# Kernel tuning notes

Hardware: AMD Instinct MI355X
Metric: run time of the kernel (lower is better)

## Reference

```python
import jax, jax.numpy as jnp
import numpy as np

N_ROIS, ROI_DIM, D, H, L, FF, NCLS = 200, 199, 192, 6, 3, 576, 2
EPS = 1e-5

def _ln(x, g, b):
    m = jnp.mean(x, axis=-1, keepdims=True)
    v = jnp.mean((x - m) ** 2, axis=-1, keepdims=True)
    return (x - m) * jax.lax.rsqrt(v + EPS) * g + b

def _gelu(x):
    return jax.nn.gelu(x, approximate=False)

def _mha(q, k, v, Wqkv, bqkv, Wo, bo):
    # q: [B,Q,D], k/v: [B,S,D]; Wqkv: [3,D,D], bqkv: [3,D]
    B, Q, _ = q.shape
    S = k.shape[1]
    Dh = D // H
    qp = (q @ Wqkv[0] + bqkv[0]).reshape(B, Q, H, Dh)
    kp = (k @ Wqkv[1] + bqkv[1]).reshape(B, S, H, Dh)
    vp = (v @ Wqkv[2] + bqkv[2]).reshape(B, S, H, Dh)
    scores = jnp.einsum('bqhd,bkhd->bhqk', qp, kp) / jnp.sqrt(jnp.float32(Dh))
    attn = jax.nn.softmax(scores, axis=-1)
    out = jnp.einsum('bhqk,bkhd->bqhd', attn, vp).reshape(B, Q, D)
    return out @ Wo + bo

def setup_inputs() -> dict:
    key = jax.random.key(0)
    ks = iter(jax.random.split(key, 40))
    r = lambda *s: jax.random.normal(next(ks), s, dtype=jnp.float32) * 0.02
    inp = {
        'x': jax.random.normal(next(ks), (256, N_ROIS * ROI_DIM), dtype=jnp.float32),
        # 200 distinct per-ROI tokenizers, stacked for a single batched GEMM
        'roi_W': r(N_ROIS, ROI_DIM, D), 'roi_b': r(N_ROIS, D),
        'roi_ln_g': jnp.ones((N_ROIS, D), jnp.float32), 'roi_ln_b': jnp.zeros((N_ROIS, D), jnp.float32),
        'pos_emb': r(N_ROIS, D),
        # encoder layers stacked on leading L dim
        'enc_Wqkv': r(L, 3, D, D), 'enc_bqkv': r(L, 3, D),
        'enc_Wo': r(L, D, D), 'enc_bo': r(L, D),
        'enc_ln1_g': jnp.ones((L, D), jnp.float32), 'enc_ln1_b': jnp.zeros((L, D), jnp.float32),
        'enc_W1': r(L, D, FF), 'enc_b1': r(L, FF),
        'enc_W2': r(L, FF, D), 'enc_b2': r(L, D),
        'enc_ln2_g': jnp.ones((L, D), jnp.float32), 'enc_ln2_b': jnp.zeros((L, D), jnp.float32),
        # attention pooling MHA
        'pool_Wqkv': r(3, D, D), 'pool_bqkv': r(3, D),
        'pool_Wo': r(D, D), 'pool_bo': r(D),
        # classifier head
        'cls_ln_g': jnp.ones((D,), jnp.float32), 'cls_ln_b': jnp.zeros((D,), jnp.float32),
        'cls_W1': r(D, D // 2), 'cls_b1': r(D // 2),
        'cls_W2': r(D // 2, D // 4), 'cls_b2': r(D // 4),
        'cls_W3': r(D // 4, NCLS), 'cls_b3': r(NCLS),
    }
    return inp

def reference(x, roi_W, roi_b, roi_ln_g, roi_ln_b, pos_emb,
              enc_Wqkv, enc_bqkv, enc_Wo, enc_bo, enc_ln1_g, enc_ln1_b,
              enc_W1, enc_b1, enc_W2, enc_b2, enc_ln2_g, enc_ln2_b,
              pool_Wqkv, pool_bqkv, pool_Wo, pool_bo,
              cls_ln_g, cls_ln_b, cls_W1, cls_b1, cls_W2, cls_b2, cls_W3, cls_b3):
    B = x.shape[0]
    roi = x.reshape(B, N_ROIS, ROI_DIM)
    # fused per-ROI Linear (200 distinct weights) as one batched GEMM
    tok = jnp.einsum('brf,rfd->brd', roi, roi_W) + roi_b  # [B,200,192]
    tok = _gelu(_ln(tok, roi_ln_g, roi_ln_b))  # dropout = identity (eval)
    tok = tok + pos_emb[None]
    # post-norm transformer encoder (PyTorch default norm_first=False)
    h = tok
    for i in range(L):
        a = _mha(h, h, h, enc_Wqkv[i], enc_bqkv[i], enc_Wo[i], enc_bo[i])
        h = _ln(h + a, enc_ln1_g[i], enc_ln1_b[i])
        f = _gelu(h @ enc_W1[i] + enc_b1[i]) @ enc_W2[i] + enc_b2[i]
        h = _ln(h + f, enc_ln2_g[i], enc_ln2_b[i])
    # MHA pooling: query = mean over ROI tokens
    q = jnp.mean(h, axis=1, keepdims=True)  # [B,1,D]
    pooled = _mha(q, h, h, pool_Wqkv, pool_bqkv, pool_Wo, pool_bo)[:, 0]  # [B,D]
    # classifier
    z = _ln(pooled, cls_ln_g, cls_ln_b)
    z = _gelu(z @ cls_W1 + cls_b1)
    z = _gelu(z @ cls_W2 + cls_b2)
    return z @ cls_W3 + cls_b3
```

## Files before the change

### kernel.cpp

```cpp
#include <hip/hip_runtime.h>
#include <math.h>


typedef unsigned short u16;
typedef unsigned int u32;
typedef __attribute__((ext_vector_type(8))) __bf16 bf16x8;
typedef __attribute__((ext_vector_type(4))) float f32x4;

#define GLL16(gp, lp) __builtin_amdgcn_global_load_lds(                 \
    (const __attribute__((address_space(1))) void*)(gp),                \
    (__attribute__((address_space(3))) void*)(lp), 16, 0, 0)

#define FENCE_VM()   do { asm volatile("s_waitcnt vmcnt(0)" ::: "memory");  \
                          __builtin_amdgcn_sched_barrier(0); } while (0)
#define FENCE_LGKM() do { asm volatile("s_waitcnt lgkmcnt(0)" ::: "memory");\
                          __builtin_amdgcn_sched_barrier(0); } while (0)

__device__ __forceinline__ u16 f2bf(float x) {
    u32 u = __float_as_uint(x);
    u = (u + 0x7FFFu + ((u >> 16) & 1u)) >> 16;
    return (u16)u;
}
__device__ __forceinline__ float bf2f(u16 h) {
    return __uint_as_float(((u32)h) << 16);
}

__device__ __forceinline__ float gelu_exact(float x) {
    return 0.5f * x * (1.0f + erff(x * 0.7071067811865475f));
}

__device__ __forceinline__ float wave_sum(float v) {
#pragma unroll
    for (int o = 32; o > 0; o >>= 1) v += __shfl_xor(v, o, 64);
    return v;
}
__device__ __forceinline__ float wave_max(float v) {
#pragma unroll
    for (int o = 32; o > 0; o >>= 1) v = fmaxf(v, __shfl_xor(v, o, 64));
    return v;
}
__device__ __forceinline__ float row_sum16(float v) {
    v += __shfl_xor(v, 1, 64); v += __shfl_xor(v, 2, 64);
    v += __shfl_xor(v, 4, 64); v += __shfl_xor(v, 8, 64);
    return v;
}

__device__ __forceinline__ f32x4 mfma_bf16(bf16x8 a, bf16x8 b, f32x4 c) {
    return __builtin_amdgcn_mfma_f32_16x16x32_bf16(a, b, c, 0, 0, 0);
}

__global__ void conv_wt(const float* __restrict__ W, u16* __restrict__ oh,
                        int K, int N)
{
    const long z = blockIdx.z;
    const int idx = blockIdx.x * 256 + threadIdx.x;
    if (idx >= K * N) return;
    const int k = idx / N, n = idx - k * N;
    const float x = W[z * K * N + idx];
    oh[z * (long)K * N + (long)n * K + k] = f2bf(x);
}

__global__ void conv_x(const float* __restrict__ x, u16* __restrict__ xh)
{
    const long idx = (long)blockIdx.x * 256 + threadIdx.x;
    if (idx >= 200L * 256 * 224) return;
    const int k = (int)(idx % 224);
    const long t = idx / 224;
    const int m = (int)(t % 256);
    const int z = (int)(t / 256);
    const float v = (k < 199) ? x[(long)m * 39800 + z * 199 + k] : 0.f;
    xh[idx] = f2bf(v);
}

__global__ void conv_roiw(const float* __restrict__ W, u16* __restrict__ oh)
{
    __shared__ float tile[32][33];
    const int z = blockIdx.z;
    const int k0 = blockIdx.x * 32;
    const int n0 = blockIdx.y * 32;
    for (int i = threadIdx.y; i < 32; i += 8) {
        const int k = k0 + i, n = n0 + threadIdx.x;
        tile[i][threadIdx.x] = (k < 199) ? W[((long)z * 199 + k) * 192 + n] : 0.f;
    }
    __syncthreads();
    for (int i = threadIdx.y; i < 32; i += 8) {
        const int n = n0 + i, k = k0 + threadIdx.x;
        const float v = tile[threadIdx.x][i];
        oh[((long)z * 192 + n) * 224 + k] = f2bf(v);
    }
}

template<int EPI>
__global__ __launch_bounds__(256, 3) void gemm_ns(
    const u16* __restrict__ Ah,
    const u16* __restrict__ Bh,
    const float* __restrict__ bias,
    float* __restrict__ C, u16* __restrict__ Ch,
    int N, int K)
{
    __shared__ u16 Ash[128][32];
    __shared__ u16 Bsh[192][32];

    const int tid = threadIdx.x;
    const int wave = tid >> 6, lane = tid & 63;
    const int lm = lane & 15, quad = lane >> 4;
    const int wm = wave >> 1, wn = wave & 1;
    const long m0 = (long)blockIdx.x * 128;
    const int n0 = blockIdx.y * 192;
    const int lrow = lane >> 2;
    const int lch  = (((lane & 3) ^ (lrow & 3)) * 8);
    const int sq   = (quad ^ (lm & 3)) * 8;

    const u16* pA0h = Ah + (m0 + wave * 32 +  0 + lrow) * K + lch;
    const u16* pA1h = Ah + (m0 + wave * 32 + 16 + lrow) * K + lch;
    const u16* pB0h = Bh + (long)(n0 + wave * 48 +  0 + lrow) * K + lch;
    const u16* pB1h = Bh + (long)(n0 + wave * 48 + 16 + lrow) * K + lch;
    const u16* pB2h = Bh + (long)(n0 + wave * 48 + 32 + lrow) * K + lch;

    auto stage = [&](int k0) {
        GLL16(pA0h + k0, &Ash[wave * 32][0]);
        GLL16(pA1h + k0, &Ash[wave * 32 + 16][0]);
        GLL16(pB0h + k0, &Bsh[wave * 48][0]);
        GLL16(pB1h + k0, &Bsh[wave * 48 + 16][0]);
        GLL16(pB2h + k0, &Bsh[wave * 48 + 32][0]);
    };

    f32x4 acc[4][6];
#pragma unroll
    for (int i = 0; i < 4; i++)
#pragma unroll
        for (int j = 0; j < 6; j++)
#pragma unroll
            for (int r = 0; r < 4; r++) acc[i][j][r] = 0.f;

    const int kt = K >> 5;
    stage(0);
    FENCE_VM();
    __syncthreads();

    for (int t = 0; t < kt; t++) {
        bf16x8 afh[4];
#pragma unroll
        for (int mi = 0; mi < 4; mi++)
            afh[mi] = *(const bf16x8*)&Ash[wm * 64 + mi * 16 + lm][sq];
#pragma unroll
        for (int jh = 0; jh < 2; jh++) {
            bf16x8 bfh[3];
#pragma unroll
            for (int j = 0; j < 3; j++)
                bfh[j] = *(const bf16x8*)&Bsh[wn * 96 + (jh * 3 + j) * 16 + lm][sq];
#pragma unroll
            for (int mi = 0; mi < 4; mi++)
#pragma unroll
                for (int j = 0; j < 3; j++)
                    acc[mi][jh * 3 + j] =
                        mfma_bf16(afh[mi], bfh[j], acc[mi][jh * 3 + j]);
        }
        if (t + 1 < kt) {
            __syncthreads();
            stage((t + 1) << 5);
            FENCE_VM();
            __syncthreads();
        }
    }

#pragma unroll
    for (int mi = 0; mi < 4; mi++) {
        const long rowb = m0 + wm * 64 + mi * 16 + quad * 4;
#pragma unroll
        for (int nj = 0; nj < 6; nj++) {
            const int col = n0 + wn * 96 + nj * 16 + lm;
            const float bv = bias[col];
#pragma unroll
            for (int r = 0; r < 4; r++) {
                float v = acc[mi][nj][r] + bv;
                if (EPI == 0) {
                    C[(rowb + r) * N + col] = v;
                } else {
                    if (EPI == 2) v = gelu_exact(v);
                    Ch[(rowb + r) * N + col] = f2bf(v);
                }
            }
        }
    }
}

__global__ __launch_bounds__(256, 3) void gemm_ln(
    const u16* __restrict__ Ah,
    const u16* __restrict__ Bh,
    const float* __restrict__ bias,
    u16* __restrict__ Hh, u16* __restrict__ Hl,
    const float* __restrict__ lng, const float* __restrict__ lnb,
    int K)
{
    __shared__ u16 Ash[128][32];
    __shared__ u16 Bsh[192][32];

    const int tid = threadIdx.x;
    const int wave = tid >> 6, lane = tid & 63;
    const int lm = lane & 15, quad = lane >> 4;
    const long m0 = (long)blockIdx.x * 128;
    const int lrow = lane >> 2;
    const int lch  = (((lane & 3) ^ (lrow & 3)) * 8);
    const int sq   = (quad ^ (lm & 3)) * 8;

    const u16* pA0h = Ah + (m0 + wave * 32 +  0 + lrow) * K + lch;
    const u16* pA1h = Ah + (m0 + wave * 32 + 16 + lrow) * K + lch;
    const u16* pB0h = Bh + (long)(wave * 48 +  0 + lrow) * K + lch;
    const u16* pB1h = Bh + (long)(wave * 48 + 16 + lrow) * K + lch;
    const u16* pB2h = Bh + (long)(wave * 48 + 32 + lrow) * K + lch;

    auto stage = [&](int k0) {
        GLL16(pA0h + k0, &Ash[wave * 32][0]);
        GLL16(pA1h + k0, &Ash[wave * 32 + 16][0]);
        GLL16(pB0h + k0, &Bsh[wave * 48][0]);
        GLL16(pB1h + k0, &Bsh[wave * 48 + 16][0]);
        GLL16(pB2h + k0, &Bsh[wave * 48 + 32][0]);
    };

    f32x4 acc[2][12];
#pragma unroll
    for (int i = 0; i < 2; i++)
#pragma unroll
        for (int j = 0; j < 12; j++)
#pragma unroll
            for (int r = 0; r < 4; r++) acc[i][j][r] = 0.f;

    const int kt = K >> 5;
    stage(0);
    FENCE_VM();
    __syncthreads();

    for (int t = 0; t < kt; t++) {
        bf16x8 afh[2];
#pragma unroll
        for (int mi = 0; mi < 2; mi++)
            afh[mi] = *(const bf16x8*)&Ash[wave * 32 + mi * 16 + lm][sq];
#pragma unroll
        for (int g = 0; g < 4; g++) {
            bf16x8 bfh[3];
#pragma unroll
            for (int j = 0; j < 3; j++)
                bfh[j] = *(const bf16x8*)&Bsh[g * 48 + j * 16 + lm][sq];
#pragma unroll
            for (int mi = 0; mi < 2; mi++)
#pragma unroll
                for (int j = 0; j < 3; j++) {
                    const int ni = g * 3 + j;
                    acc[mi][ni] = mfma_bf16(afh[mi], bfh[j], acc[mi][ni]);
                }
        }
        if (t + 1 < kt) {
            __syncthreads();
            stage((t + 1) << 5);
            FENCE_VM();
            __syncthreads();
        }
    }

    float gv[12], bv2[12], biasv[12];
#pragma unroll
    for (int ni = 0; ni < 12; ni++) {
        const int col = ni * 16 + lm;
        gv[ni] = lng[col]; bv2[ni] = lnb[col]; biasv[ni] = bias[col];
    }
#pragma unroll
    for (int mi = 0; mi < 2; mi++) {
#pragma unroll
        for (int r = 0; r < 4; r++) {
            const long row = m0 + wave * 32 + mi * 16 + quad * 4 + r;
            const long rb = row * 192;
            float vals[12];
            float s = 0.f;
#pragma unroll
            for (int ni = 0; ni < 12; ni++) {
                const int col = ni * 16 + lm;
                const float hval = bf2f(Hh[rb + col]) + bf2f(Hl[rb + col]);
                vals[ni] = acc[mi][ni][r] + biasv[ni] + hval;
                s += vals[ni];
            }
            const float mean = row_sum16(s) * (1.f / 192.f);
            float ss = 0.f;
#pragma unroll
            for (int ni = 0; ni < 12; ni++) {
                vals[ni] -= mean;
                ss += vals[ni] * vals[ni];
            }
            const float var = row_sum16(ss) * (1.f / 192.f);
            const float rsr = 1.f / sqrtf(var + 1e-5f);
#pragma unroll
            for (int ni = 0; ni < 12; ni++) {
                const int col = ni * 16 + lm;
                const float y = vals[ni] * rsr * gv[ni] + bv2[ni];
                const u16 hb = f2bf(y);
                Hh[rb + col] = hb;
                Hl[rb + col] = f2bf(y - bf2f(hb));
            }
        }
    }
}

__global__ __launch_bounds__(256, 3) void tok_mfma(
    const u16* __restrict__ xh,
    const u16* __restrict__ wth,
    const float* __restrict__ roi_b,
    const float* __restrict__ lng, const float* __restrict__ lnb,
    const float* __restrict__ pos,
    u16* __restrict__ hh, u16* __restrict__ hl)
{
    __shared__ u16 Ash[128][32];
    __shared__ u16 Bsh[192][32];

    const int tid = threadIdx.x;
    const int wave = tid >> 6, lane = tid & 63;
    const int lm = lane & 15, quad = lane >> 4;
    const int m0 = blockIdx.x * 128;
    const int z = blockIdx.y;
    const int lrow = lane >> 2;
    const int lch  = (((lane & 3) ^ (lrow & 3)) * 8);
    const int sq   = (quad ^ (lm & 3)) * 8;
    const int K = 224;

    const u16* pA0h = xh + ((long)z * 256 + m0 + wave * 32 +  0 + lrow) * K + lch;
    const u16* pA1h = xh + ((long)z * 256 + m0 + wave * 32 + 16 + lrow) * K + lch;
    const u16* pB0h = wth + ((long)z * 192 + wave * 48 +  0 + lrow) * K + lch;
    const u16* pB1h = wth + ((long)z * 192 + wave * 48 + 16 + lrow) * K + lch;
    const u16* pB2h = wth + ((long)z * 192 + wave * 48 + 32 + lrow) * K + lch;

    auto stage = [&](int k0) {
        GLL16(pA0h + k0, &Ash[wave * 32][0]);
        GLL16(pA1h + k0, &Ash[wave * 32 + 16][0]);
        GLL16(pB0h + k0, &Bsh[wave * 48][0]);
        GLL16(pB1h + k0, &Bsh[wave * 48 + 16][0]);
        GLL16(pB2h + k0, &Bsh[wave * 48 + 32][0]);
    };

    f32x4 acc[2][12];
#pragma unroll
    for (int i = 0; i < 2; i++)
#pragma unroll
        for (int j = 0; j < 12; j++)
#pragma unroll
            for (int r = 0; r < 4; r++) acc[i][j][r] = 0.f;

    stage(0);
    FENCE_VM();
    __syncthreads();
    for (int t = 0; t < 7; t++) {
        bf16x8 afh[2];
#pragma unroll
        for (int mi = 0; mi < 2; mi++)
            afh[mi] = *(const bf16x8*)&Ash[wave * 32 + mi * 16 + lm][sq];
#pragma unroll
        for (int g = 0; g < 4; g++) {
            bf16x8 bfh[3];
#pragma unroll
            for (int j = 0; j < 3; j++)
                bfh[j] = *(const bf16x8*)&Bsh[g * 48 + j * 16 + lm][sq];
#pragma unroll
            for (int mi = 0; mi < 2; mi++)
#pragma unroll
                for (int j = 0; j < 3; j++) {
                    const int ni = g * 3 + j;
                    acc[mi][ni] = mfma_bf16(afh[mi], bfh[j], acc[mi][ni]);
                }
        }
        if (t + 1 < 7) {
            __syncthreads();
            stage((t + 1) << 5);
            FENCE_VM();
            __syncthreads();
        }
    }

    float gv[12], bv2[12], biasv[12], pv[12];
#pragma unroll
    for (int ni = 0; ni < 12; ni++) {
        const int col = ni * 16 + lm;
        gv[ni]    = lng[z * 192 + col];
        bv2[ni]   = lnb[z * 192 + col];
        biasv[ni] = roi_b[z * 192 + col];
        pv[ni]    = pos[z * 192 + col];
    }
#pragma unroll
    for (int mi = 0; mi < 2; mi++) {
#pragma unroll
        for (int r = 0; r < 4; r++) {
            const int brow = m0 + wave * 32 + mi * 16 + quad * 4 + r;
            float vals[12];
            float s = 0.f;
#pragma unroll
            for (int ni = 0; ni < 12; ni++) {
                vals[ni] = acc[mi][ni][r] + biasv[ni];
                s += vals[ni];
            }
            const float mean = row_sum16(s) * (1.f / 192.f);
            float ss = 0.f;
#pragma unroll
            for (int ni = 0; ni < 12; ni++) {
                vals[ni] -= mean;
                ss += vals[ni] * vals[ni];
            }
            const float var = row_sum16(ss) * (1.f / 192.f);
            const float rsr = 1.f / sqrtf(var + 1e-5f);
            const long ob = ((long)brow * 200 + z) * 192;
#pragma unroll
            for (int ni = 0; ni < 12; ni++) {
                const int col = ni * 16 + lm;
                const float y = gelu_exact(vals[ni] * rsr * gv[ni] + bv2[ni]) + pv[ni];
                const u16 hb = f2bf(y);
                hh[ob + col] = hb;
                hl[ob + col] = f2bf(y - bf2f(hb));
            }
        }
    }
}

template<int EPI>
__global__ __launch_bounds__(256) void gemm_kernel(
    const float* __restrict__ A, int lda, long strideA,
    const float* __restrict__ Bw, long strideB,
    const float* __restrict__ bias, long strideBias,
    float* __restrict__ C, int ldc, long strideC,
    int M, int N, int K, int ldb)
{
    __shared__ float As[16][132];
    __shared__ float Bs[16][68];

    const int z = blockIdx.z;
    const float* Ab    = A    + (long)z * strideA;
    const float* Bb    = Bw   + (long)z * strideB;
    const float* biasb = bias + (long)z * strideBias;
    float*       Cb    = C    + (long)z * strideC;

    const int row0 = blockIdx.x * 128;
    const int col0 = blockIdx.y * 64;
    const int tid  = threadIdx.x;
    const int tm = tid >> 4;
    const int tn = tid & 15;

    const int la_m = tid >> 1;
    const int la_k = (tid & 1) * 8;
    const int lb_k = tid >> 4;
    const int lb_n = (tid & 15) * 4;

    const float* bcol = Bb + (col0 + lb_n);
    const float* arow = Ab + (long)(row0 + la_m) * lda;
    const bool vecA = ((lda & 3) == 0) &&
                      ((((unsigned long long)(const void*)arow) & 15ull) == 0ull);

    float acc[8][4];
#pragma unroll
    for (int i = 0; i < 8; i++)
#pragma unroll
        for (int j = 0; j < 4; j++) acc[i][j] = 0.f;

    for (int k0 = 0; k0 < K; k0 += 16) {
        if (vecA && (k0 + 16 <= K)) {
            float4 v0 = *(const float4*)(arow + k0 + la_k);
            float4 v1 = *(const float4*)(arow + k0 + la_k + 4);
            As[la_k + 0][la_m] = v0.x; As[la_k + 1][la_m] = v0.y;
            As[la_k + 2][la_m] = v0.z; As[la_k + 3][la_m] = v0.w;
            As[la_k + 4][la_m] = v1.x; As[la_k + 5][la_m] = v1.y;
            As[la_k + 6][la_m] = v1.z; As[la_k + 7][la_m] = v1.w;
        } else {
#pragma unroll
            for (int i = 0; i < 8; i++) {
                int k = k0 + la_k + i;
                As[la_k + i][la_m] = (k < K) ? arow[k] : 0.f;
            }
        }
        {
            int k = k0 + lb_k;
            float4 v = make_float4(0.f, 0.f, 0.f, 0.f);
            if (k < K) v = *(const float4*)(bcol + (long)k * ldb);
            *(float4*)&Bs[lb_k][lb_n] = v;
        }
        __syncthreads();
#pragma unroll
        for (int kk = 0; kk < 16; kk++) {
            float4 a0 = *(const float4*)&As[kk][tm * 8];
            float4 a1 = *(const float4*)&As[kk][tm * 8 + 4];
            float4 b4 = *(const float4*)&Bs[kk][tn * 4];
            float av[8] = {a0.x, a0.y, a0.z, a0.w, a1.x, a1.y, a1.z, a1.w};
            float bv[4] = {b4.x, b4.y, b4.z, b4.w};
#pragma unroll
            for (int i = 0; i < 8; i++)
#pragma unroll
                for (int j = 0; j < 4; j++) acc[i][j] += av[i] * bv[j];
        }
        __syncthreads();
    }

    const int gcol = col0 + tn * 4;
    float4 bv4 = *(const float4*)(biasb + gcol);
#pragma unroll
    for (int i = 0; i < 8; i++) {
        int grow = row0 + tm * 8 + i;
        float4 o;
        o.x = acc[i][0] + bv4.x; o.y = acc[i][1] + bv4.y;
        o.z = acc[i][2] + bv4.z; o.w = acc[i][3] + bv4.w;
        if (EPI == 1) {
            o.x = gelu_exact(o.x); o.y = gelu_exact(o.y);
            o.z = gelu_exact(o.z); o.w = gelu_exact(o.w);
        }
        *(float4*)(Cb + (long)grow * ldc + gcol) = o;
    }
}

__global__ __launch_bounds__(256, 2) void attn_enc_mfma(
    const u16* __restrict__ qkvh, u16* __restrict__ outh)
{
    __shared__ u16 Ksh[96][40];
    __shared__ u16 Vth[32][104];
    __shared__ u16 Pbuf[4][2][16][40];

    const int bh = blockIdx.x;
    const int b = bh / 6, h = bh % 6;
    const int tid = threadIdx.x;
    const int wave = tid >> 6, lane = tid & 63;
    const int lm = lane & 15, quad = lane >> 4;
    const int nq = (wave == 0) ? 4 : 3;

    uint4 qh[4];
#pragma unroll
    for (int i = 0; i < 4; i++) {
        if (i < nq) {
            int qt = wave + 4 * i;
            int qrow = qt * 16 + lm; if (qrow > 199) qrow = 199;
            const long off = (long)(b * 200 + qrow) * 576 + h * 32 + quad * 8;
            qh[i] = *(const uint4*)(qkvh + off);
        }
    }

    float mrow[4][4], lrow[4][4];
    f32x4 accO[4][2];
#pragma unroll
    for (int i = 0; i < 4; i++)
#pragma unroll
        for (int r = 0; r < 4; r++) {
            mrow[i][r] = -1e30f; lrow[i][r] = 0.f;
            accO[i][0][r] = 0.f; accO[i][1][r] = 0.f;
        }

    const float scale = 0.17677669529663688f;
    int par = 0;

#pragma unroll
    for (int ph = 0; ph < 3; ph++) {
        const int base = (ph == 0) ? 0 : (ph == 1) ? 96 : 192;
        const int ntl  = (ph == 2) ? 2 : 6;
        const int nslot = ntl * 16;

        __syncthreads();
        if (wave < 2) {
            const int sub = wave * 64 + lane;
#pragma unroll
            for (int rep = 0; rep < 3; rep++) {
                const int idx = rep * 128 + sub;
                if (idx < nslot * 4) {
                    const int key = idx >> 2, ch = idx & 3;
                    const int gk = base + key;
                    const bool valid = gk < 200;
                    const long roff = (long)(b * 200 + (valid ? gk : 0)) * 576
                                      + h * 32 + 192 + ch * 8;
                    uint4 v = valid ? *(const uint4*)(qkvh + roff)
                                    : make_uint4(0, 0, 0, 0);
                    *(uint4*)(&Ksh[0][0] + key * 40 + ch * 8) = v;
                }
            }
        } else {
            const int sub = (wave - 2) * 64 + lane;
#pragma unroll
            for (int rep = 0; rep < 2; rep++) {
                const int idx = rep * 128 + sub;
                if (idx < nslot * 2) {
                    const int key = idx >> 1, hf = idx & 1;
                    const int gk = base + key;
                    const bool valid = gk < 200;
                    const long roff = (long)(b * 200 + (valid ? gk : 0)) * 576
                                      + h * 32 + 384 + hf * 16;
                    uint4 v0 = valid ? *(const uint4*)(qkvh + roff)
                                     : make_uint4(0, 0, 0, 0);
                    uint4 v1 = valid ? *(const uint4*)(qkvh + roff + 8)
                                     : make_uint4(0, 0, 0, 0);
                    const u16* p0 = (const u16*)&v0;
                    const u16* p1 = (const u16*)&v1;
#pragma unroll
                    for (int j = 0; j < 8; j++) {
                        Vth[hf * 16 + j][key]     = p0[j];
                        Vth[hf * 16 + 8 + j][key] = p1[j];
                    }
                }
            }
        }
        __syncthreads();

#pragma unroll
        for (int i = 0; i < 4; i++) {
            if (i >= nq) continue;
            const bf16x8 qhf = *(const bf16x8*)&qh[i];
            float s[6][4];
#pragma unroll
            for (int ni = 0; ni < 6; ni++) {
                if (ni >= ntl) continue;
                bf16x8 kh8 = *(const bf16x8*)&Ksh[ni * 16 + lm][quad * 8];
                f32x4 c = {0.f, 0.f, 0.f, 0.f};
                c = mfma_bf16(qhf, kh8, c);
                const bool masked = (base + ni * 16 + lm) >= 200;
#pragma unroll
                for (int r = 0; r < 4; r++)
                    s[ni][r] = masked ? -1e30f : c[r] * scale;
            }
            float fac[4];
#pragma unroll
            for (int r = 0; r < 4; r++) {
                float pm = s[0][r];
#pragma unroll
                for (int ni = 1; ni < 6; ni++)
                    if (ni < ntl) pm = fmaxf(pm, s[ni][r]);
                pm = fmaxf(pm, __shfl_xor(pm, 1, 64));
                pm = fmaxf(pm, __shfl_xor(pm, 2, 64));
                pm = fmaxf(pm, __shfl_xor(pm, 4, 64));
                pm = fmaxf(pm, __shfl_xor(pm, 8, 64));
                const float mn = fmaxf(mrow[i][r], pm);
                fac[r] = __expf(mrow[i][r] - mn);
                mrow[i][r] = mn;
                float ps = 0.f;
#pragma unroll
                for (int ni = 0; ni < 6; ni++) {
                    if (ni >= ntl) continue;
                    float e = __expf(s[ni][r] - mn);
                    s[ni][r] = e;
                    ps += e;
                }
                ps += __shfl_xor(ps, 1, 64);
                ps += __shfl_xor(ps, 2, 64);
                ps += __shfl_xor(ps, 4, 64);
                ps += __shfl_xor(ps, 8, 64);
                lrow[i][r] = lrow[i][r] * fac[r] + ps;
                accO[i][0][r] *= fac[r];
                accO[i][1][r] *= fac[r];
            }
#pragma unroll
            for (int ck = 0; ck < 3; ck++) {
                if (ck >= (ntl >> 1)) continue;
                const int pb = par & 1; par++;
#pragma unroll
                for (int tl = 0; tl < 2; tl++) {
#pragma unroll
                    for (int r = 0; r < 4; r++) {
                        Pbuf[wave][pb][quad * 4 + r][tl * 16 + lm] =
                            f2bf(s[2 * ck + tl][r]);
                    }
                }
                FENCE_LGKM();
                const bf16x8 pa = *(const bf16x8*)&Pbuf[wave][pb][lm][quad * 8];
#pragma unroll
                for (int nt = 0; nt < 2; nt++) {
                    bf16x8 vh8 = *(const bf16x8*)&Vth[nt * 16 + lm][ck * 32 + quad * 8];
                    accO[i][nt] = mfma_bf16(pa, vh8, accO[i][nt]);
                }
            }
        }
    }

#pragma unroll
    for (int i = 0; i < 4; i++) {
        if (i >= nq) continue;
        const int qt = wave + 4 * i;
#pragma unroll
        for (int r = 0; r < 4; r++) {
            const int qrow = qt * 16 + quad * 4 + r;
            if (qrow >= 200) continue;
            const float inv = 1.f / lrow[i][r];
            const long ob = (long)(b * 200 + qrow) * 192 + h * 32 + lm;
            outh[ob]      = f2bf(accO[i][0][r] * inv);
            outh[ob + 16] = f2bf(accO[i][1][r] * inv);
        }
    }
}

__global__ __launch_bounds__(192) void mean_tokens_pair(
    const u16* __restrict__ hh, const u16* __restrict__ hl, float* __restrict__ qmean)
{
    const int b = blockIdx.x, d = threadIdx.x;
    float s = 0.f;
    for (int r = 0; r < 200; r++) {
        const long idx = ((long)b * 200 + r) * 192 + d;
        s += bf2f(hh[idx]) + bf2f(hl[idx]);
    }
    qmean[b * 192 + d] = s * (1.f / 200.f);
}

__global__ __launch_bounds__(64) void attn_pool(
    const float* __restrict__ qp, const float* __restrict__ kv,
    float* __restrict__ out)
{
    __shared__ float p[200];
    const int b = blockIdx.x / 6, h = blockIdx.x % 6;
    const int lane = threadIdx.x;

    const float* qrow = qp + b * 192 + h * 32;
    float qr[32];
#pragma unroll
    for (int u = 0; u < 8; u++) {
        float4 t = *(const float4*)(qrow + 4 * u);
        qr[4 * u] = t.x; qr[4 * u + 1] = t.y;
        qr[4 * u + 2] = t.z; qr[4 * u + 3] = t.w;
    }
    const float scale = 0.17677669529663688f;
    const float* kb = kv + (long)(b * 200) * 384 + h * 32;
    float s[4];
    float mymax = -1e30f;
#pragma unroll
    for (int g = 0; g < 4; g++) {
        int j = lane + 64 * g;
        if (j < 200) {
            const float* kr = kb + (long)j * 384;
            float acc = 0.f;
#pragma unroll
            for (int u = 0; u < 8; u++) {
                float4 k4 = *(const float4*)(kr + 4 * u);
                acc += qr[4 * u] * k4.x + qr[4 * u + 1] * k4.y +
                       qr[4 * u + 2] * k4.z + qr[4 * u + 3] * k4.w;
            }
            s[g] = acc * scale;
            mymax = fmaxf(mymax, s[g]);
        } else {
            s[g] = -1e30f;
        }
    }
    float mx = wave_max(mymax);
    float psum = 0.f;
#pragma unroll
    for (int g = 0; g < 4; g++) {
        int j = lane + 64 * g;
        if (j < 200) {
            float e = __expf(s[g] - mx);
            p[j] = e;
            psum += e;
        }
    }
    float tot = wave_sum(psum);
    __syncthreads();
    const int half = lane >> 5, d = lane & 31;
    const float* vb = kv + (long)(b * 200) * 384 + 192 + h * 32 + d;
    float acc = 0.f;
    for (int jj = 0; jj < 100; jj++) {
        int j = half * 100 + jj;
        acc += p[j] * vb[(long)j * 384];
    }
    acc += __shfl_xor(acc, 32, 64);
    acc /= tot;
    if (lane < 32) out[b * 192 + h * 32 + d] = acc;
}

__global__ __launch_bounds__(64) void classifier_kernel(
    const float* __restrict__ pooled,
    const float* __restrict__ g, const float* __restrict__ bt,
    const float* __restrict__ W1, const float* __restrict__ b1,
    const float* __restrict__ W2, const float* __restrict__ b2,
    const float* __restrict__ W3, const float* __restrict__ b3,
    float* __restrict__ out)
{
    __shared__ float z[192];
    __shared__ float z1[96];
    __shared__ float z2[48];
    const int b = blockIdx.x, lane = threadIdx.x;
    const float* pr = pooled + b * 192;
    float x0 = pr[lane], x1 = pr[lane + 64], x2 = pr[lane + 128];
    float m = wave_sum(x0 + x1 + x2) * (1.f / 192.f);
    float d0 = x0 - m, d1 = x1 - m, d2 = x2 - m;
    float v = wave_sum(d0 * d0 + d1 * d1 + d2 * d2) * (1.f / 192.f);
    float rs = 1.f / sqrtf(v + 1e-5f);
    z[lane]       = d0 * rs * g[lane]       + bt[lane];
    z[lane + 64]  = d1 * rs * g[lane + 64]  + bt[lane + 64];
    z[lane + 128] = d2 * rs * g[lane + 128] + bt[lane + 128];
    __syncthreads();
#pragma unroll
    for (int rep = 0; rep < 2; rep++) {
        int j = lane + rep * 64;
        if (j < 96) {
            float a = b1[j];
            for (int k = 0; k < 192; k++) a += z[k] * W1[k * 96 + j];
            z1[j] = gelu_exact(a);
        }
    }
    __syncthreads();
    if (lane < 48) {
        float a = b2[lane];
        for (int k = 0; k < 96; k++) a += z1[k] * W2[k * 48 + lane];
        z2[lane] = gelu_exact(a);
    }
    __syncthreads();
    if (lane < 2) {
        float a = b3[lane];
        for (int k = 0; k < 48; k++) a += z2[k] * W3[k * 2 + lane];
        out[b * 2 + lane] = a;
    }
}

extern "C" void kernel_launch(void* const* d_in, const int* in_sizes, int n_in,
                              void* d_out, int out_size, void* d_ws, size_t ws_size,
                              hipStream_t stream)
{
    (void)in_sizes; (void)n_in; (void)out_size; (void)ws_size;

    const float* x         = (const float*)d_in[0];
    const float* roi_W     = (const float*)d_in[1];
    const float* roi_b     = (const float*)d_in[2];
    const float* roi_ln_g  = (const float*)d_in[3];
    const float* roi_ln_b  = (const float*)d_in[4];
    const float* pos_emb   = (const float*)d_in[5];
    const float* enc_Wqkv  = (const float*)d_in[6];
    const float* enc_bqkv  = (const float*)d_in[7];
    const float* enc_Wo    = (const float*)d_in[8];
    const float* enc_bo    = (const float*)d_in[9];
    const float* enc_ln1_g = (const float*)d_in[10];
    const float* enc_ln1_b = (const float*)d_in[11];
    const float* enc_W1    = (const float*)d_in[12];
    const float* enc_b1    = (const float*)d_in[13];
    const float* enc_W2    = (const float*)d_in[14];
    const float* enc_b2    = (const float*)d_in[15];
    const float* enc_ln2_g = (const float*)d_in[16];
    const float* enc_ln2_b = (const float*)d_in[17];
    const float* pool_Wqkv = (const float*)d_in[18];
    const float* pool_bqkv = (const float*)d_in[19];
    const float* pool_Wo   = (const float*)d_in[20];
    const float* pool_bo   = (const float*)d_in[21];
    const float* cls_ln_g  = (const float*)d_in[22];
    const float* cls_ln_b  = (const float*)d_in[23];
    const float* cls_W1    = (const float*)d_in[24];
    const float* cls_b1    = (const float*)d_in[25];
    const float* cls_W2    = (const float*)d_in[26];
    const float* cls_b2    = (const float*)d_in[27];
    const float* cls_W3    = (const float*)d_in[28];
    const float* cls_b3    = (const float*)d_in[29];

    char* ws = (char*)d_ws;
    u16*   hh    = (u16*)(ws);
    u16*   hl    = (u16*)(ws + 19660800);
    char*  bufA  = ws + 39321600;
    float* bufAf = (float*)bufA;
    u16*   xh    = (u16*)bufA;
    u16*   wth   = (u16*)(bufA + 45875200);
    u16*   qkvh  = (u16*)bufA;
    u16*   ffh   = (u16*)bufA;
    char*  bufB  = ws + 157286400;
    u16*   bBh   = (u16*)bufB;
    float* qmean = (float*)(ws + 196608000);
    float* qp    = qmean + 49152;
    float* pattn = qp + 49152;
    float* pooled= pattn + 49152;
    char*  wts   = ws + 197394432;
    u16* WqkvH = (u16*)(wts);
    u16* Wff1H = (u16*)(wts + 1327104);
    u16* Wff2H = (u16*)(wts + 2654208);
    u16* WwoH  = (u16*)(wts + 3981312);
    u16* WkvH  = (u16*)(wts + 4423680);

    conv_wt<<<dim3(144, 1, 9), 256, 0, stream>>>(enc_Wqkv, WqkvH, 192, 192);
    conv_wt<<<dim3(432, 1, 3), 256, 0, stream>>>(enc_W1, Wff1H, 192, 576);
    conv_wt<<<dim3(432, 1, 3), 256, 0, stream>>>(enc_W2, Wff2H, 576, 192);
    conv_wt<<<dim3(144, 1, 3), 256, 0, stream>>>(enc_Wo, WwoH, 192, 192);
    conv_wt<<<dim3(144, 1, 2), 256, 0, stream>>>(pool_Wqkv + 36864, WkvH, 192, 192);

    conv_x<<<44800, 256, 0, stream>>>(x, xh);
    conv_roiw<<<dim3(7, 6, 200), dim3(32, 8), 0, stream>>>(roi_W, wth);
    tok_mfma<<<dim3(2, 200), 256, 0, stream>>>(
        xh, wth, roi_b, roi_ln_g, roi_ln_b, pos_emb, hh, hl);

    for (int i = 0; i < 3; i++) {
        gemm_ns<3><<<dim3(400, 3), 256, 0, stream>>>(
            hh, WqkvH + (long)i * 110592,
            enc_bqkv + i * 576, nullptr, qkvh, 576, 192);
        attn_enc_mfma<<<1536, 256, 0, stream>>>(qkvh, bBh);
        gemm_ln<<<dim3(400, 1), 256, 0, stream>>>(
            bBh, WwoH + (long)i * 36864,
            enc_bo + i * 192,
            hh, hl, enc_ln1_g + i * 192, enc_ln1_b + i * 192, 192);
        gemm_ns<2><<<dim3(400, 3), 256, 0, stream>>>(
            hh, Wff1H + (long)i * 110592,
            enc_b1 + i * 576, nullptr, ffh, 576, 192);
        gemm_ln<<<dim3(400, 1), 256, 0, stream>>>(
            ffh, Wff2H + (long)i * 110592,
            enc_b2 + i * 192,
            hh, hl, enc_ln2_g + i * 192, enc_ln2_b + i * 192, 576);
    }

    mean_tokens_pair<<<256, 192, 0, stream>>>(hh, hl, qmean);
    gemm_kernel<0><<<dim3(2, 3, 1), 256, 0, stream>>>(
        qmean, 192, 0, pool_Wqkv, 0, pool_bqkv, 0, qp, 192, 0, 256, 192, 192, 192);
    gemm_ns<0><<<dim3(400, 2), 256, 0, stream>>>(
        hh, WkvH, pool_bqkv + 192, bufAf, nullptr, 384, 192);
    attn_pool<<<1536, 64, 0, stream>>>(qp, bufAf, pattn);
    gemm_kernel<0><<<dim3(2, 3, 1), 256, 0, stream>>>(
        pattn, 192, 0, pool_Wo, 0, pool_bo, 0, pooled, 192, 0, 256, 192, 192, 192);

    classifier_kernel<<<256, 64, 0, stream>>>(
        pooled, cls_ln_g, cls_ln_b,
        cls_W1, cls_b1, cls_W2, cls_b2, cls_W3, cls_b3,
        (float*)d_out);
}
```

Baseline: 937.3 us.

## Load full K/V per head into LDS and use single-pass softmax

The encoder attention kernel now stages all 200 keys and values for a (batch, head) into shared memory at once, instead of three chunked phases with online-softmax rescaling. Each query tile computes all 13 score tiles, takes an exact max and sum, then accumulates P·V over 7 chunks. This removes two block barriers, the repeated staging loops and the rescale arithmetic. In exchange it uses more LDS and more registers for the 13x4 score array, which may lower occupancy.

```diff
diff --git a/kernel.cpp b/kernel.cpp
--- a/kernel.cpp
+++ b/kernel.cpp
@@ -511,8 +511,8 @@
 __global__ __launch_bounds__(256, 2) void attn_enc_mfma(
     const u16* __restrict__ qkvh, u16* __restrict__ outh)
 {
-    __shared__ u16 Ksh[96][40];
-    __shared__ u16 Vth[32][104];
+    __shared__ u16 Ksh[208][40];
+    __shared__ u16 Vth[32][224];
     __shared__ u16 Pbuf[4][2][16][40];
 
     const int bh = blockIdx.x;
@@ -533,134 +533,109 @@
         }
     }
 
-    float mrow[4][4], lrow[4][4];
-    f32x4 accO[4][2];
-#pragma unroll
-    for (int i = 0; i < 4; i++)
-#pragma unroll
-        for (int r = 0; r < 4; r++) {
-            mrow[i][r] = -1e30f; lrow[i][r] = 0.f;
-            accO[i][0][r] = 0.f; accO[i][1][r] = 0.f;
-        }
+    if (wave < 2) {
+        const int sub = wave * 64 + lane;
+#pragma unroll
+        for (int rep = 0; rep < 7; rep++) {
+            const int idx = rep * 128 + sub;
+            if (idx < 208 * 4) {
+                const int key = idx >> 2, ch = idx & 3;
+                const bool valid = key < 200;
+                const long roff = (long)(b * 200 + (valid ? key : 0)) * 576
+                                  + h * 32 + 192 + ch * 8;
+                uint4 v = valid ? *(const uint4*)(qkvh + roff)
+                                : make_uint4(0, 0, 0, 0);
+                *(uint4*)(&Ksh[0][0] + key * 40 + ch * 8) = v;
+            }
+        }
+    } else {
+        const int sub = (wave - 2) * 64 + lane;
+#pragma unroll
+        for (int rep = 0; rep < 4; rep++) {
+            const int idx = rep * 128 + sub;
+            if (idx < 224 * 2) {
+                const int key = idx >> 1, hf = idx & 1;
+                const bool valid = key < 200;
+                const long roff = (long)(b * 200 + (valid ? key : 0)) * 576
+                                  + h * 32 + 384 + hf * 16;
+                uint4 v0 = valid ? *(const uint4*)(qkvh + roff)
+                                 : make_uint4(0, 0, 0, 0);
+                uint4 v1 = valid ? *(const uint4*)(qkvh + roff + 8)
+                                 : make_uint4(0, 0, 0, 0);
+                const u16* p0 = (const u16*)&v0;
+                const u16* p1 = (const u16*)&v1;
+#pragma unroll
+                for (int j = 0; j < 8; j++) {
+                    Vth[hf * 16 + j][key]     = p0[j];
+                    Vth[hf * 16 + 8 + j][key] = p1[j];
+                }
+            }
+        }
+    }
+    __syncthreads();
 
     const float scale = 0.17677669529663688f;
     int par = 0;
-
-#pragma unroll
-    for (int ph = 0; ph < 3; ph++) {
-        const int base = (ph == 0) ? 0 : (ph == 1) ? 96 : 192;
-        const int ntl  = (ph == 2) ? 2 : 6;
-        const int nslot = ntl * 16;
-
-        __syncthreads();
-        if (wave < 2) {
-            const int sub = wave * 64 + lane;
-#pragma unroll
-            for (int rep = 0; rep < 3; rep++) {
-                const int idx = rep * 128 + sub;
-                if (idx < nslot * 4) {
-                    const int key = idx >> 2, ch = idx & 3;
-                    const int gk = base + key;
-                    const bool valid = gk < 200;
-                    const long roff = (long)(b * 200 + (valid ? gk : 0)) * 576
-                                      + h * 32 + 192 + ch * 8;
-                    uint4 v = valid ? *(const uint4*)(qkvh + roff)
-                                    : make_uint4(0, 0, 0, 0);
-                    *(uint4*)(&Ksh[0][0] + key * 40 + ch * 8) = v;
+    float lrow[4][4];
+    f32x4 accO[4][2];
+
+#pragma unroll
+    for (int i = 0; i < 4; i++) {
+        if (i >= nq) continue;
+        const bf16x8 qhf = *(const bf16x8*)&qh[i];
+        float s[13][4];
+#pragma unroll
+        for (int ni = 0; ni < 13; ni++) {
+            bf16x8 kh8 = *(const bf16x8*)&Ksh[ni * 16 + lm][quad * 8];
+            f32x4 c = {0.f, 0.f, 0.f, 0.f};
+            c = mfma_bf16(qhf, kh8, c);
+            const bool masked = (ni * 16 + lm) >= 200;
+#pragma unroll
+            for (int r = 0; r < 4; r++)
+                s[ni][r] = masked ? -1e30f : c[r] * scale;
+        }
+#pragma unroll
+        for (int r = 0; r < 4; r++) {
+            float pm = s[0][r];
+#pragma unroll
+            for (int ni = 1; ni < 13; ni++) pm = fmaxf(pm, s[ni][r]);
+            pm = fmaxf(pm, __shfl_xor(pm, 1, 64));
+            pm = fmaxf(pm, __shfl_xor(pm, 2, 64));
+            pm = fmaxf(pm, __shfl_xor(pm, 4, 64));
+            pm = fmaxf(pm, __shfl_xor(pm, 8, 64));
+            float ps = 0.f;
+#pragma unroll
+            for (int ni = 0; ni < 13; ni++) {
+                float e = __expf(s[ni][r] - pm);
+                s[ni][r] = e;
+                ps += e;
+            }
+            ps += __shfl_xor(ps, 1, 64);
+            ps += __shfl_xor(ps, 2, 64);
+            ps += __shfl_xor(ps, 4, 64);
+            ps += __shfl_xor(ps, 8, 64);
+            lrow[i][r] = ps;
+            accO[i][0][r] = 0.f;
+            accO[i][1][r] = 0.f;
+        }
+#pragma unroll
+        for (int ck = 0; ck < 7; ck++) {
+            const int pb = par & 1; par++;
+#pragma unroll
+            for (int tl = 0; tl < 2; tl++) {
+                const int t = 2 * ck + tl;
+#pragma unroll
+                for (int r = 0; r < 4; r++) {
+                    const float val = (t < 13) ? s[t][r] : 0.f;
+                    Pbuf[wave][pb][quad * 4 + r][tl * 16 + lm] = f2bf(val);
                 }
             }
-        } else {
-            const int sub = (wave - 2) * 64 + lane;
-#pragma unroll
-            for (int rep = 0; rep < 2; rep++) {
-                const int idx = rep * 128 + sub;
-                if (idx < nslot * 2) {
-                    const int key = idx >> 1, hf = idx & 1;
-                    const int gk = base + key;
-                    const bool valid = gk < 200;
-                    const long roff = (long)(b * 200 + (valid ? gk : 0)) * 576
-                                      + h * 32 + 384 + hf * 16;
-                    uint4 v0 = valid ? *(const uint4*)(qkvh + roff)
-                                     : make_uint4(0, 0, 0, 0);
-                    uint4 v1 = valid ? *(const uint4*)(qkvh + roff + 8)
-                                     : make_uint4(0, 0, 0, 0);
-                    const u16* p0 = (const u16*)&v0;
-                    const u16* p1 = (const u16*)&v1;
-#pragma unroll
-                    for (int j = 0; j < 8; j++) {
-                        Vth[hf * 16 + j][key]     = p0[j];
-                        Vth[hf * 16 + 8 + j][key] = p1[j];
-                    }
-                }
-            }
-        }
-        __syncthreads();
-
-#pragma unroll
-        for (int i = 0; i < 4; i++) {
-            if (i >= nq) continue;
-            const bf16x8 qhf = *(const bf16x8*)&qh[i];
-            float s[6][4];
-#pragma unroll
-            for (int ni = 0; ni < 6; ni++) {
-                if (ni >= ntl) continue;
-                bf16x8 kh8 = *(const bf16x8*)&Ksh[ni * 16 + lm][quad * 8];
-                f32x4 c = {0.f, 0.f, 0.f, 0.f};
-                c = mfma_bf16(qhf, kh8, c);
-                const bool masked = (base + ni * 16 + lm) >= 200;
-#pragma unroll
-                for (int r = 0; r < 4; r++)
-                    s[ni][r] = masked ? -1e30f : c[r] * scale;
-            }
-            float fac[4];
-#pragma unroll
-            for (int r = 0; r < 4; r++) {
-                float pm = s[0][r];
-#pragma unroll
-                for (int ni = 1; ni < 6; ni++)
-                    if (ni < ntl) pm = fmaxf(pm, s[ni][r]);
-                pm = fmaxf(pm, __shfl_xor(pm, 1, 64));
-                pm = fmaxf(pm, __shfl_xor(pm, 2, 64));
-                pm = fmaxf(pm, __shfl_xor(pm, 4, 64));
-                pm = fmaxf(pm, __shfl_xor(pm, 8, 64));
-                const float mn = fmaxf(mrow[i][r], pm);
-                fac[r] = __expf(mrow[i][r] - mn);
-                mrow[i][r] = mn;
-                float ps = 0.f;
-#pragma unroll
-                for (int ni = 0; ni < 6; ni++) {
-                    if (ni >= ntl) continue;
-                    float e = __expf(s[ni][r] - mn);
-                    s[ni][r] = e;
-                    ps += e;
-                }
-                ps += __shfl_xor(ps, 1, 64);
-                ps += __shfl_xor(ps, 2, 64);
-                ps += __shfl_xor(ps, 4, 64);
-                ps += __shfl_xor(ps, 8, 64);
-                lrow[i][r] = lrow[i][r] * fac[r] + ps;
-                accO[i][0][r] *= fac[r];
-                accO[i][1][r] *= fac[r];
-            }
-#pragma unroll
-            for (int ck = 0; ck < 3; ck++) {
-                if (ck >= (ntl >> 1)) continue;
-                const int pb = par & 1; par++;
-#pragma unroll
-                for (int tl = 0; tl < 2; tl++) {
-#pragma unroll
-                    for (int r = 0; r < 4; r++) {
-                        Pbuf[wave][pb][quad * 4 + r][tl * 16 + lm] =
-                            f2bf(s[2 * ck + tl][r]);
-                    }
-                }
-                FENCE_LGKM();
-                const bf16x8 pa = *(const bf16x8*)&Pbuf[wave][pb][lm][quad * 8];
-#pragma unroll
-                for (int nt = 0; nt < 2; nt++) {
-                    bf16x8 vh8 = *(const bf16x8*)&Vth[nt * 16 + lm][ck * 32 + quad * 8];
-                    accO[i][nt] = mfma_bf16(pa, vh8, accO[i][nt]);
-                }
+            FENCE_LGKM();
+            const bf16x8 pa = *(const bf16x8*)&Pbuf[wave][pb][lm][quad * 8];
+#pragma unroll
+            for (int nt = 0; nt < 2; nt++) {
+                bf16x8 vh8 = *(const bf16x8*)&Vth[nt * 16 + lm][ck * 32 + quad * 8];
+                accO[i][nt] = mfma_bf16(pa, vh8, accO[i][nt]);
             }
         }
     }
```

New measurement: 873.1 us. -6.9%, faster.
